# Kernel tuning notes

Measured on AMD Instinct MI355X. Metric: run time of the kernel, lower is better.

The kernel has to match this reference:

```python
import jax, jax.numpy as jnp
import numpy as np

B, S, D = 2, 1024, 2048
H, HKV, HD = 16, 8, 128
F, E, R = 5632, 8, 16
EPS = 1e-5
SCALE = 2.0  # lora_alpha / r = 32 / 16


def _rope_tables():
    pos = jnp.arange(S, dtype=jnp.float32)
    inv = 1.0 / (10000.0 ** (jnp.arange(0, HD, 2, dtype=jnp.float32) / HD))
    ang = pos[:, None] * inv[None, :]  # [S, HD/2]
    return jnp.cos(ang), jnp.sin(ang)


def setup_inputs() -> dict:
    key = jax.random.key(0)
    ks = jax.random.split(key, 18)
    p = lambda k, shp: jax.random.normal(k, shp, dtype=jnp.float32) * 0.02
    cos, sin = _rope_tables()
    return {
        'data': jax.random.normal(ks[0], (B, S, D), dtype=jnp.float32),
        'mask': jnp.zeros((1, 1, S, S), dtype=jnp.float32),
        'rope_cos': cos,
        'rope_sin': sin,
        'attn_norm_w': jnp.ones((D,), jnp.float32),
        'ffn_norm_w': jnp.ones((D,), jnp.float32),
        'wq': p(ks[1], (D, D)),
        'wk': p(ks[2], (HKV * HD, D)),
        'wv': p(ks[3], (HKV * HD, D)),
        'wo': p(ks[4], (D, D)),
        'gate_w': p(ks[5], (E, D)),
        'w1': p(ks[6], (F, D)),
        'w2': p(ks[7], (D, F)),
        'w3': p(ks[8], (F, D)),
        'w1_a': p(ks[9], (E, R, D)),
        'w1_b': p(ks[10], (E, F, R)),
        'w3_a': p(ks[11], (E, R, D)),
        'w3_b': p(ks[12], (E, F, R)),
        'w2_a': p(ks[13], (E, R, F)),
        'w2_b': p(ks[14], (E, D, R)),
    }


def _rmsnorm(x, w):
    v = jnp.mean(x.astype(jnp.float32) ** 2, axis=-1, keepdims=True)
    return (x * jax.lax.rsqrt(v + EPS)).astype(x.dtype) * w


def _rope(x, cos, sin):
    # x: [B,S,h,HD]; interleaved-pair rotation (llama apply_rotary_emb)
    x1, x2 = x[..., 0::2], x[..., 1::2]
    c, s = cos[None, :, None, :], sin[None, :, None, :]
    o1 = x1 * c - x2 * s
    o2 = x1 * s + x2 * c
    return jnp.stack([o1, o2], axis=-1).reshape(x.shape)


def reference(data, mask, rope_cos, rope_sin, attn_norm_w, ffn_norm_w,
              wq, wk, wv, wo, gate_w, w1, w2, w3,
              w1_a, w1_b, w3_a, w3_b, w2_a, w2_b):
    # ---- attention block ----
    xn = _rmsnorm(data, attn_norm_w)
    q = (xn @ wq.T).reshape(B, S, H, HD)
    k = (xn @ wk.T).reshape(B, S, HKV, HD)
    v = (xn @ wv.T).reshape(B, S, HKV, HD)
    q = _rope(q, rope_cos, rope_sin)
    k = _rope(k, rope_cos, rope_sin)
    k = jnp.repeat(k, H // HKV, axis=2)  # repeat_kv
    v = jnp.repeat(v, H // HKV, axis=2)
    scores = jnp.einsum('bqhd,bkhd->bhqk', q, k) / np.float32(np.sqrt(HD)) + mask
    probs = jax.nn.softmax(scores, axis=-1)
    attn = jnp.einsum('bhqk,bkhd->bqhd', probs, v).reshape(B, S, H * HD)
    data = data + attn @ wo.T
    # ---- MoE block ----
    sn = _rmsnorm(data, ffn_norm_w)
    logits = sn @ gate_w.T  # [B,S,E]
    # NOTE: source uses F.softmax(..., dim=1) -> softmax over SEQ axis, replicated faithfully
    rw = jax.nn.softmax(logits.astype(jnp.float32), axis=1)
    rw, sel = jax.lax.top_k(rw, 2)  # over experts (last axis)
    rw = rw / jnp.sum(rw, axis=-1, keepdims=True)
    c1 = sn @ w1.T  # [B,S,F]
    c3 = sn @ w3.T
    acc = jnp.zeros_like(data)
    for e in range(E):  # dense per-expert loop, as in source
        h1 = c1 + ((sn @ w1_a[e].T) @ w1_b[e].T) * SCALE
        h3 = c3 + ((sn @ w3_a[e].T) @ w3_b[e].T) * SCALE
        sr = jax.nn.silu(h1) * h3
        h = sr @ w2.T + ((sr @ w2_a[e].T) @ w2_b[e].T) * SCALE
        ew = jnp.sum(rw * (sel == e), axis=-1, keepdims=True).astype(h.dtype)
        acc = acc + h * ew
    return data + acc
```

## Files before the change

### kernel.cpp

```cpp
#include <hip/hip_runtime.h>
#include <hip/hip_bf16.h>
#include <stdint.h>

#define DEVI __device__ __forceinline__

typedef __attribute__((ext_vector_type(8))) short short8;
typedef __attribute__((ext_vector_type(4))) short short4b;
typedef __attribute__((ext_vector_type(4))) float f32x4;

constexpr int Bb  = 2, Ss = 1024, Dd = 2048, Hh = 16, HKVv = 8, HDd = 128;
constexpr int Ff  = 5632, Ee = 8, Rr = 16;
constexpr int Tt  = Bb * Ss;
constexpr int M2  = 2 * Tt;
constexpr int NKV = HKVv * HDd;
constexpr int NQKV = Dd + 2 * NKV;
constexpr int F2  = 2 * Ff;

DEVI unsigned short f2bf(float f) {
  union { float f; unsigned u; } x; x.f = f;
  unsigned r = (x.u + 0x7FFFu + ((x.u >> 16) & 1u)) >> 16;
  return (unsigned short)r;
}
DEVI float bf2f(unsigned short h) {
  union { unsigned u; float f; } x; x.u = ((unsigned)h) << 16; return x.f;
}
DEVI float wsum64(float v) {
  #pragma unroll
  for (int d = 1; d < 64; d <<= 1) v += __shfl_xor(v, d, 64);
  return v;
}
DEVI float wsum16(float v) {
  v += __shfl_xor(v, 1, 64); v += __shfl_xor(v, 2, 64);
  v += __shfl_xor(v, 4, 64); v += __shfl_xor(v, 8, 64);
  return v;
}
DEVI float wmax16(float v) {
  v = fmaxf(v, __shfl_xor(v, 1, 64)); v = fmaxf(v, __shfl_xor(v, 2, 64));
  v = fmaxf(v, __shfl_xor(v, 4, 64)); v = fmaxf(v, __shfl_xor(v, 8, 64));
  return v;
}
typedef __attribute__((address_space(1))) void gvoid;
typedef __attribute__((address_space(3))) void lvoid;
DEVI void gl_lds16(const void* g, void* l) {
  __builtin_amdgcn_global_load_lds((gvoid*)g, (lvoid*)l, 16, 0, 0);
}
DEVI unsigned ldsoff(const void* p) {
  return (unsigned)(uintptr_t)(lvoid*)p;
}
DEVI f32x4 mfma16x16(short8 a, short8 b, f32x4 c) {
  return __builtin_amdgcn_mfma_f32_16x16x32_bf16(a, b, c, 0, 0, 0);
}

__global__ __launch_bounds__(256) void cast_w(const float* __restrict__ in,
                                              unsigned short* __restrict__ out, int n) {
  int i = (blockIdx.x * 256 + threadIdx.x) * 8;
  if (i >= n) return;
  const float4* p = (const float4*)(in + i);
  float4 a = p[0], b = p[1];
  float v[8] = {a.x,a.y,a.z,a.w,b.x,b.y,b.z,b.w};
  short8 o;
  #pragma unroll
  for (int j = 0; j < 8; ++j) o[j] = (short)f2bf(v[j]);
  *(short8*)(out + i) = o;
}
__global__ __launch_bounds__(256) void cast_split_w(const float* __restrict__ in,
                                                    unsigned short* __restrict__ oh,
                                                    unsigned short* __restrict__ ol, int n) {
  int i = (blockIdx.x * 256 + threadIdx.x) * 8;
  if (i >= n) return;
  const float4* p = (const float4*)(in + i);
  float4 a = p[0], b = p[1];
  float v[8] = {a.x,a.y,a.z,a.w,b.x,b.y,b.z,b.w};
  short8 h, l;
  #pragma unroll
  for (int j = 0; j < 8; ++j) {
    unsigned short hb = f2bf(v[j]);
    h[j] = (short)hb;
    l[j] = (short)f2bf(v[j] - bf2f(hb));
  }
  *(short8*)(oh + i) = h;
  *(short8*)(ol + i) = l;
}
__global__ __launch_bounds__(256) void zero_f32(float* __restrict__ p, int n) {
  int i = blockIdx.x * 256 + threadIdx.x;
  if (i < n) p[i] = 0.f;
}

__global__ __launch_bounds__(256) void rmsnorm_k(const float* __restrict__ x,
                                                 const float* __restrict__ w,
                                                 unsigned short* __restrict__ out) {
  int row = blockIdx.x, tid = threadIdx.x;
  const float* xr = x + (size_t)row * Dd;
  const float4* p4 = (const float4*)(xr + tid * 8);
  float4 a = p4[0], b = p4[1];
  float v[8] = {a.x,a.y,a.z,a.w,b.x,b.y,b.z,b.w};
  float ss = 0.f;
  #pragma unroll
  for (int j = 0; j < 8; ++j) ss += v[j] * v[j];
  ss = wsum64(ss);
  __shared__ float red[4];
  int wv_ = tid >> 6, l = tid & 63;
  if (l == 0) red[wv_] = ss;
  __syncthreads();
  float tot = red[0] + red[1] + red[2] + red[3];
  float rstd = rsqrtf(tot * (1.0f / Dd) + 1e-5f);
  const float* wr = w + tid * 8;
  short8 o;
  #pragma unroll
  for (int j = 0; j < 8; ++j) o[j] = (short)f2bf(v[j] * rstd * wr[j]);
  *(short8*)(out + (size_t)row * Dd + tid * 8) = o;
}

__global__ __launch_bounds__(256) void rmsnorm_split_k(const float* __restrict__ x,
                                                       const float* __restrict__ w,
                                                       unsigned short* __restrict__ outh,
                                                       unsigned short* __restrict__ outl) {
  int row = blockIdx.x, tid = threadIdx.x;
  const float* xr = x + (size_t)row * Dd;
  const float4* p4 = (const float4*)(xr + tid * 8);
  float4 a = p4[0], b = p4[1];
  float v[8] = {a.x,a.y,a.z,a.w,b.x,b.y,b.z,b.w};
  float ss = 0.f;
  #pragma unroll
  for (int j = 0; j < 8; ++j) ss += v[j] * v[j];
  ss = wsum64(ss);
  __shared__ float red[4];
  int wv_ = tid >> 6, l = tid & 63;
  if (l == 0) red[wv_] = ss;
  __syncthreads();
  float tot = red[0] + red[1] + red[2] + red[3];
  float rstd = rsqrtf(tot * (1.0f / Dd) + 1e-5f);
  const float* wr = w + tid * 8;
  short8 oh, ol;
  #pragma unroll
  for (int j = 0; j < 8; ++j) {
    float val = v[j] * rstd * wr[j];
    unsigned short hb = f2bf(val);
    oh[j] = (short)hb;
    ol[j] = (short)f2bf(val - bf2f(hb));
  }
  *(short8*)(outh + (size_t)row * Dd + tid * 8) = oh;
  *(short8*)(outl + (size_t)row * Dd + tid * 8) = ol;
}

template <int MODE, int COLMAJ>
__global__ __launch_bounds__(512) void gemm_bt64_v3(const unsigned short* __restrict__ A,
                                                    const unsigned short* __restrict__ Bw,
                                                    void* __restrict__ C0,
                                                    void* __restrict__ C1,
                                                    int M, int N, int Kext, int ld, int gx) {
  __shared__ __align__(16) unsigned short As[128 * 64];
  __shared__ __align__(16) unsigned short Bs[128 * 64];
  int tid = threadIdx.x;
  int w = tid >> 6, l = tid & 63;
  int lr = l & 15, lg = l >> 4;
  int cpx = (int)gridDim.x >> 3;
  int bid = blockIdx.x;
  int swz = (bid & 7) * cpx + (bid >> 3);
  int mtiles = M >> 7;
  int bx, by, ks = 0;
  if (COLMAJ) { by = swz % mtiles; bx = swz / mtiles; }
  else {
    bx = swz % gx; by = swz / gx;
    if (by >= mtiles) { ks = 1; by -= mtiles; }
  }
  int m0 = by * 128, n0 = bx * 128;
  int koff = ks * Kext;
  int wr = (w >> 1) * 32, wc = (w & 1) * 64;
  f32x4 acc[2][4];
  #pragma unroll
  for (int i = 0; i < 2; ++i)
    #pragma unroll
    for (int j = 0; j < 4; ++j) acc[i][j] = (f32x4){0.f, 0.f, 0.f, 0.f};

  int srow = w * 16 + (l >> 3);
  int schunk = (l & 7) ^ (l >> 3);
  const unsigned short* ga = A  + (size_t)(m0 + srow) * ld + koff + schunk * 8;
  const unsigned short* gb = Bw + (size_t)(n0 + srow) * ld + koff + schunk * 8;
  unsigned short* lA = As + w * 1024;
  unsigned short* lB = Bs + w * 1024;

  for (int k0 = 0; k0 < Kext; k0 += 64) {
    #pragma unroll
    for (int c = 0; c < 2; ++c) {
      gl_lds16(ga + k0 + (size_t)(c * 8) * ld, lA + c * 512);
      gl_lds16(gb + k0 + (size_t)(c * 8) * ld, lB + c * 512);
    }
    __syncthreads();
    #pragma unroll
    for (int kk = 0; kk < 2; ++kk) {
      int rc = ((kk * 4 + lg) ^ (lr & 7)) * 8;
      short8 af[2], bfr[4];
      #pragma unroll
      for (int i = 0; i < 2; ++i)
        af[i]  = *(const short8*)(As + (wr + i * 16 + lr) * 64 + rc);
      #pragma unroll
      for (int j = 0; j < 4; ++j)
        bfr[j] = *(const short8*)(Bs + (wc + j * 16 + lr) * 64 + rc);
      #pragma unroll
      for (int i = 0; i < 2; ++i)
        #pragma unroll
        for (int j = 0; j < 4; ++j) acc[i][j] = mfma16x16(af[i], bfr[j], acc[i][j]);
    }
    __syncthreads();
  }
  float* Cf = (float*)(ks ? C1 : C0);
  #pragma unroll
  for (int i = 0; i < 2; ++i)
    #pragma unroll
    for (int j = 0; j < 4; ++j) {
      int m = m0 + wr + i * 16 + lg * 4;
      int n = n0 + wc + j * 16 + lr;
      #pragma unroll
      for (int r = 0; r < 4; ++r) {
        float vv = acc[i][j][r];
        size_t o = (size_t)(m + r) * N + n;
        if (MODE == 0) ((unsigned short*)C0)[o] = f2bf(vv);
        else           Cf[o] = vv;
      }
    }
}

template <int MODE, int COLMAJ>
__global__ __launch_bounds__(512) void gemm3_v3(const unsigned short* __restrict__ Ah,
                                                const unsigned short* __restrict__ Al,
                                                const unsigned short* __restrict__ Bh1,
                                                const unsigned short* __restrict__ Bl1,
                                                const unsigned short* __restrict__ Bh2,
                                                const unsigned short* __restrict__ Bl2,
                                                const unsigned short* __restrict__ Bh3,
                                                const unsigned short* __restrict__ Bl3,
                                                int nsplit1, int nsplit2,
                                                void* __restrict__ C0,
                                                const float* __restrict__ resid,
                                                int M, int N, int K, int gx) {
  __shared__ __align__(16) unsigned short Ash[128 * 32];
  __shared__ __align__(16) unsigned short Asl[128 * 32];
  __shared__ __align__(16) unsigned short Bsh[128 * 32];
  __shared__ __align__(16) unsigned short Bsl[128 * 32];
  int tid = threadIdx.x;
  int w = tid >> 6, l = tid & 63;
  int lr = l & 15, lg = l >> 4;
  int cpx = (int)gridDim.x >> 3;
  int bid = blockIdx.x;
  int swz = (bid & 7) * cpx + (bid >> 3);
  int mtiles = M >> 7;
  int bx, by;
  if (COLMAJ) { by = swz % mtiles; bx = swz / mtiles; }
  else        { bx = swz % gx;     by = swz / gx; }
  int m0 = by * 128, n0 = bx * 128;
  int wr = (w >> 1) * 32, wc = (w & 1) * 64;

  const unsigned short* Bh; const unsigned short* Bl; int nb;
  if (n0 < nsplit1)      { Bh = Bh1; Bl = Bl1; nb = n0; }
  else if (n0 < nsplit2) { Bh = Bh2; Bl = Bl2; nb = n0 - nsplit1; }
  else                   { Bh = Bh3; Bl = Bl3; nb = n0 - nsplit2; }

  f32x4 acc[2][4];
  #pragma unroll
  for (int i = 0; i < 2; ++i)
    #pragma unroll
    for (int j = 0; j < 4; ++j) acc[i][j] = (f32x4){0.f, 0.f, 0.f, 0.f};

  int srow = w * 16 + (l >> 2);
  int scol = ((l & 3) ^ ((l >> 3) & 3)) * 8;
  const unsigned short* gah = Ah + (size_t)(m0 + srow) * K + scol;
  const unsigned short* gal = Al + (size_t)(m0 + srow) * K + scol;
  const unsigned short* gbh = Bh + (size_t)(nb + srow) * K + scol;
  const unsigned short* gbl = Bl + (size_t)(nb + srow) * K + scol;
  unsigned short* lAh = Ash + w * 512;
  unsigned short* lAl = Asl + w * 512;
  unsigned short* lBh = Bsh + w * 512;
  unsigned short* lBl = Bsl + w * 512;

  for (int k0 = 0; k0 < K; k0 += 32) {
    gl_lds16(gah + k0, lAh);
    gl_lds16(gal + k0, lAl);
    gl_lds16(gbh + k0, lBh);
    gl_lds16(gbl + k0, lBl);
    __syncthreads();
    int rc = (lg ^ ((lr >> 1) & 3)) * 8;
    short8 afh[2], afl[2], bfh[4], bfl[4];
    #pragma unroll
    for (int i = 0; i < 2; ++i) {
      afh[i] = *(const short8*)(Ash + (wr + i * 16 + lr) * 32 + rc);
      afl[i] = *(const short8*)(Asl + (wr + i * 16 + lr) * 32 + rc);
    }
    #pragma unroll
    for (int j = 0; j < 4; ++j) {
      bfh[j] = *(const short8*)(Bsh + (wc + j * 16 + lr) * 32 + rc);
      bfl[j] = *(const short8*)(Bsl + (wc + j * 16 + lr) * 32 + rc);
    }
    #pragma unroll
    for (int i = 0; i < 2; ++i)
      #pragma unroll
      for (int j = 0; j < 4; ++j) {
        acc[i][j] = mfma16x16(afh[i], bfh[j], acc[i][j]);
        acc[i][j] = mfma16x16(afh[i], bfl[j], acc[i][j]);
        acc[i][j] = mfma16x16(afl[i], bfh[j], acc[i][j]);
      }
    __syncthreads();
  }
  #pragma unroll
  for (int i = 0; i < 2; ++i)
    #pragma unroll
    for (int j = 0; j < 4; ++j) {
      int m = m0 + wr + i * 16 + lg * 4;
      int n = n0 + wc + j * 16 + lr;
      #pragma unroll
      for (int r = 0; r < 4; ++r) {
        float vv = acc[i][j][r];
        size_t o = (size_t)(m + r) * N + n;
        if (MODE == 1) ((float*)C0)[o] = vv;
        else           ((float*)C0)[o] = vv + resid[o];
      }
    }
}

__global__ __launch_bounds__(128) void vsplit_k(const float* __restrict__ qkv,
                                                unsigned short* __restrict__ vh,
                                                unsigned short* __restrict__ vl) {
  int row = blockIdx.x;
  int bas = threadIdx.x * 8;
  const float4* p = (const float4*)(qkv + (size_t)row * NQKV + Dd + NKV + bas);
  float4 a = p[0], b = p[1];
  float v[8] = {a.x,a.y,a.z,a.w,b.x,b.y,b.z,b.w};
  short8 h, l;
  #pragma unroll
  for (int j = 0; j < 8; ++j) {
    unsigned short hb = f2bf(v[j]);
    h[j] = (short)hb;
    l[j] = (short)f2bf(v[j] - bf2f(hb));
  }
  size_t o = (size_t)row * NKV + bas;
  *(short8*)(vh + o) = h;
  *(short8*)(vl + o) = l;
}

__global__ void rope_split_k(const float* __restrict__ x, int xstride,
                             const float* __restrict__ cs, const float* __restrict__ sn,
                             unsigned short* __restrict__ oh, unsigned short* __restrict__ ol,
                             int nh) {
  int row = blockIdx.x;
  int s = row & (Ss - 1);
  int nelem = nh * HDd;
  int bas = threadIdx.x * 8;
  if (bas >= nelem) return;
  const float4* px = (const float4*)(x + (size_t)row * xstride + bas);
  float4 a = px[0], b = px[1];
  float vv[8] = {a.x,a.y,a.z,a.w,b.x,b.y,b.z,b.w};
  int d = bas & (HDd - 1);
  const float* cr = cs + s * 64 + (d >> 1);
  const float* sr = sn + s * 64 + (d >> 1);
  short8 hs, ls;
  #pragma unroll
  for (int p = 0; p < 4; ++p) {
    float x1 = vv[2 * p], x2 = vv[2 * p + 1];
    float c = cr[p], si = sr[p];
    float o1 = x1 * c - x2 * si;
    float o2 = x1 * si + x2 * c;
    unsigned short h1 = f2bf(o1), h2 = f2bf(o2);
    hs[2 * p] = (short)h1;      hs[2 * p + 1] = (short)h2;
    ls[2 * p] = (short)f2bf(o1 - bf2f(h1));
    ls[2 * p + 1] = (short)f2bf(o2 - bf2f(h2));
  }
  size_t o = (size_t)row * nelem + bas;
  *(short8*)(oh + o) = hs;
  *(short8*)(ol + o) = ls;
}

__global__ __launch_bounds__(256) void attn3_k(const unsigned short* __restrict__ qh,
                                               const unsigned short* __restrict__ ql,
                                               const unsigned short* __restrict__ kh,
                                               const unsigned short* __restrict__ kl,
                                               const unsigned short* __restrict__ vh,
                                               const unsigned short* __restrict__ vl,
                                               const float* __restrict__ mask,
                                               unsigned short* __restrict__ aoh,
                                               unsigned short* __restrict__ aol) {
  __shared__ __align__(16) unsigned short Ksh[32 * 128], Ksl[32 * 128];
  __shared__ __align__(16) unsigned short VTh[8 * 528], VTl[8 * 528];
  __shared__ __align__(16) unsigned short Plh[4 * 16 * 40], Pll[4 * 16 * 40];
  int tid = threadIdx.x, w = tid >> 6, l = tid & 63;
  int lr = l & 15, lg = l >> 4;
  int b = blockIdx.y >> 4, h = blockIdx.y & 15, hk = h >> 1;
  int q0 = blockIdx.x * 64 + w * 16;

  short8 qfh[4], qfl[4];
  {
    size_t qoff = ((size_t)((b * Ss + q0 + lr) * Hh + h)) * HDd;
    #pragma unroll
    for (int ds = 0; ds < 4; ++ds) {
      qfh[ds] = *(const short8*)(qh + qoff + ds * 32 + lg * 8);
      qfl[ds] = *(const short8*)(ql + qoff + ds * 32 + lg * 8);
    }
  }

  float mreg[4] = {-1e30f, -1e30f, -1e30f, -1e30f};
  float lreg[4] = {0.f, 0.f, 0.f, 0.f};
  f32x4 oacc[8];
  #pragma unroll
  for (int db = 0; db < 8; ++db) oacc[db] = (f32x4){0.f, 0.f, 0.f, 0.f};

  const float sc = 0.08838834764831845f;
  size_t kvbase = ((size_t)(b * Ss) * HKVv + hk) * HDd;
  const unsigned short* kb_h = kh + kvbase;
  const unsigned short* kb_l = kl + kvbase;
  const unsigned short* vb_h = vh + kvbase;
  const unsigned short* vb_l = vl + kvbase;

  int kc1 = (lr ^ lg) * 8;
  int kc2 = (lr ^ (lg + 4)) * 8;
  int vrow_a = w * 8 + ((l & 7) >> 1);
  int vchunk = ((l >> 3) * 2 + (l & 1)) * 8;
  unsigned short* vh1 = VTh + (2 * w) * 528;
  unsigned short* vh2 = VTh + (2 * w + 1) * 528;
  unsigned short* vl1 = VTl + (2 * w) * 528;
  unsigned short* vl2 = VTl + (2 * w + 1) * 528;
  unsigned vtbh = ldsoff(VTh) + (unsigned)lr * 8u;
  unsigned vtbl = ldsoff(VTl) + (unsigned)lr * 8u;

  for (int kv0 = 0; kv0 < Ss; kv0 += 32) {
    int r1 = kv0 + w * 8 + lg;
    gl_lds16(kb_h + (size_t)r1 * NKV + kc1,       Ksh + w * 1024);
    gl_lds16(kb_h + (size_t)(r1 + 4) * NKV + kc2, Ksh + w * 1024 + 512);
    gl_lds16(kb_l + (size_t)r1 * NKV + kc1,       Ksl + w * 1024);
    gl_lds16(kb_l + (size_t)(r1 + 4) * NKV + kc2, Ksl + w * 1024 + 512);
    int vr0 = kv0 + vrow_a;
    gl_lds16(vb_h + (size_t)vr0 * NKV + vchunk,       vh1);
    gl_lds16(vb_h + (size_t)(vr0 + 4) * NKV + vchunk, vh2);
    gl_lds16(vb_l + (size_t)vr0 * NKV + vchunk,       vl1);
    gl_lds16(vb_l + (size_t)(vr0 + 4) * NKV + vchunk, vl2);
    __syncthreads();

    f32x4 s0 = (f32x4){0.f,0.f,0.f,0.f}, s1 = (f32x4){0.f,0.f,0.f,0.f};
    #pragma unroll
    for (int ds = 0; ds < 4; ++ds) {
      int kcol = ((ds * 4 + lg) ^ (lr & 7)) * 8;
      short8 kh0 = *(const short8*)(Ksh + lr * 128 + kcol);
      short8 kh1 = *(const short8*)(Ksh + (16 + lr) * 128 + kcol);
      short8 kl0 = *(const short8*)(Ksl + lr * 128 + kcol);
      short8 kl1 = *(const short8*)(Ksl + (16 + lr) * 128 + kcol);
      s0 = mfma16x16(qfh[ds], kh0, s0);
      s0 = mfma16x16(qfh[ds], kl0, s0);
      s0 = mfma16x16(qfl[ds], kh0, s0);
      s1 = mfma16x16(qfh[ds], kh1, s1);
      s1 = mfma16x16(qfh[ds], kl1, s1);
      s1 = mfma16x16(qfl[ds], kh1, s1);
    }
    const float* mrow = mask + (size_t)(q0 + lg * 4) * Ss + kv0 + lr;
    #pragma unroll
    for (int r = 0; r < 4; ++r) {
      float a0 = s0[r] * sc + mrow[(size_t)r * Ss];
      float a1 = s1[r] * sc + mrow[(size_t)r * Ss + 16];
      float t = wmax16(fmaxf(a0, a1));
      float mn = fmaxf(mreg[r], t);
      float resc = __expf(mreg[r] - mn);
      mreg[r] = mn;
      float e0 = __expf(a0 - mn), e1 = __expf(a1 - mn);
      float ps = wsum16(e0 + e1);
      lreg[r] = lreg[r] * resc + ps;
      #pragma unroll
      for (int db = 0; db < 8; ++db) oacc[db][r] *= resc;
      unsigned short h0 = f2bf(e0), h1 = f2bf(e1);
      unsigned short* prowh = Plh + (w * 16 + lg * 4 + r) * 40;
      unsigned short* prowl = Pll + (w * 16 + lg * 4 + r) * 40;
      prowh[lr] = h0;            prowh[16 + lr] = h1;
      prowl[lr] = f2bf(e0 - bf2f(h0));
      prowl[16 + lr] = f2bf(e1 - bf2f(h1));
    }
    asm volatile("" ::: "memory");
    short8 pfh = *(const short8*)(Plh + (w * 16 + lr) * 40 + lg * 8);
    short8 pfl = *(const short8*)(Pll + (w * 16 + lr) * 40 + lg * 8);

    short4b v4[16];
    #pragma unroll
    for (int db = 0; db < 8; ++db) {
      #pragma unroll
      for (int t = 0; t < 2; ++t) {
        unsigned off = vtbh + (unsigned)((lg * 2 + t) * 1056 + db * 128);
        asm volatile("ds_read_b64_tr_b16 %0, %1" : "=v"(v4[db * 2 + t]) : "v"(off));
      }
    }
    asm volatile("s_waitcnt lgkmcnt(0)" ::: "memory");
    __builtin_amdgcn_sched_barrier(0);
    #pragma unroll
    for (int db = 0; db < 8; ++db) {
      short8 vf;
      vf[0] = v4[db*2][0]; vf[1] = v4[db*2][1]; vf[2] = v4[db*2][2]; vf[3] = v4[db*2][3];
      vf[4] = v4[db*2+1][0]; vf[5] = v4[db*2+1][1]; vf[6] = v4[db*2+1][2]; vf[7] = v4[db*2+1][3];
      oacc[db] = mfma16x16(pfh, vf, oacc[db]);
      oacc[db] = mfma16x16(pfl, vf, oacc[db]);
    }
    #pragma unroll
    for (int db = 0; db < 8; ++db) {
      #pragma unroll
      for (int t = 0; t < 2; ++t) {
        unsigned off = vtbl + (unsigned)((lg * 2 + t) * 1056 + db * 128);
        asm volatile("ds_read_b64_tr_b16 %0, %1" : "=v"(v4[db * 2 + t]) : "v"(off));
      }
    }
    asm volatile("s_waitcnt lgkmcnt(0)" ::: "memory");
    __builtin_amdgcn_sched_barrier(0);
    #pragma unroll
    for (int db = 0; db < 8; ++db) {
      short8 vf;
      vf[0] = v4[db*2][0]; vf[1] = v4[db*2][1]; vf[2] = v4[db*2][2]; vf[3] = v4[db*2][3];
      vf[4] = v4[db*2+1][0]; vf[5] = v4[db*2+1][1]; vf[6] = v4[db*2+1][2]; vf[7] = v4[db*2+1][3];
      oacc[db] = mfma16x16(pfh, vf, oacc[db]);
    }
    __syncthreads();
  }
  float inv[4];
  #pragma unroll
  for (int r = 0; r < 4; ++r) inv[r] = 1.0f / lreg[r];
  size_t obase = ((size_t)((b * Ss + q0 + lg * 4) * Hh + h)) * HDd + lr;
  #pragma unroll
  for (int db = 0; db < 8; ++db)
    #pragma unroll
    for (int r = 0; r < 4; ++r) {
      float val = oacc[db][r] * inv[r];
      unsigned short hb = f2bf(val);
      size_t o = obase + (size_t)r * Hh * HDd + db * 16;
      aoh[o] = hb;
      aol[o] = f2bf(val - bf2f(hb));
    }
}

__global__ __launch_bounds__(256) void router_logits(const float* __restrict__ x2,
                                                     const float* __restrict__ fnw,
                                                     const float* __restrict__ gw,
                                                     float* __restrict__ logits) {
  int wid = (blockIdx.x * 256 + threadIdx.x) >> 6;
  int l = threadIdx.x & 63;
  if (wid >= Tt) return;
  const float* row = x2 + (size_t)wid * Dd;
  float xs[32]; float ss = 0.f;
  #pragma unroll
  for (int c = 0; c < 32; ++c) { float t = row[c * 64 + l]; xs[c] = t; ss += t * t; }
  ss = wsum64(ss);
  float rstd = rsqrtf(ss * (1.0f / Dd) + 1e-5f);
  #pragma unroll
  for (int c = 0; c < 32; ++c) xs[c] *= rstd * fnw[c * 64 + l];
  for (int e = 0; e < 8; ++e) {
    float a = 0.f;
    #pragma unroll
    for (int c = 0; c < 32; ++c) a += xs[c] * gw[(size_t)e * Dd + c * 64 + l];
    a = wsum64(a);
    if (l == 0) logits[wid * 8 + e] = a;
  }
}
__global__ __launch_bounds__(256) void router_colstats(const float* __restrict__ logits,
                                                       float* __restrict__ mz) {
  int b = blockIdx.x >> 3, e = blockIdx.x & 7;
  int tid = threadIdx.x, wv_ = tid >> 6, l = tid & 63;
  __shared__ float red[4];
  float mx = -1e30f;
  for (int s = tid; s < Ss; s += 256) mx = fmaxf(mx, logits[(size_t)(b * Ss + s) * 8 + e]);
  #pragma unroll
  for (int d = 1; d < 64; d <<= 1) mx = fmaxf(mx, __shfl_xor(mx, d, 64));
  if (l == 0) red[wv_] = mx;
  __syncthreads();
  mx = fmaxf(fmaxf(red[0], red[1]), fmaxf(red[2], red[3]));
  __syncthreads();
  float z = 0.f;
  for (int s = tid; s < Ss; s += 256) z += expf(logits[(size_t)(b * Ss + s) * 8 + e] - mx);
  z = wsum64(z);
  if (l == 0) red[wv_] = z;
  __syncthreads();
  if (tid == 0) {
    mz[(b * 8 + e) * 2] = mx;
    mz[(b * 8 + e) * 2 + 1] = red[0] + red[1] + red[2] + red[3];
  }
}
__global__ __launch_bounds__(256) void router_select(const float* __restrict__ logits,
                                                     const float* __restrict__ mz,
                                                     int* __restrict__ sel,
                                                     float* __restrict__ ewt) {
  int t = blockIdx.x * 256 + threadIdx.x;
  if (t >= Tt) return;
  int b = t >> 10;
  float rw[8];
  #pragma unroll
  for (int e = 0; e < 8; ++e)
    rw[e] = expf(logits[(size_t)t * 8 + e] - mz[(b * 8 + e) * 2]) / mz[(b * 8 + e) * 2 + 1];
  int i0 = 0; float b0 = rw[0];
  #pragma unroll
  for (int e = 1; e < 8; ++e) if (rw[e] > b0) { b0 = rw[e]; i0 = e; }
  int i1 = -1; float b1 = -1.f;
  #pragma unroll
  for (int e = 0; e < 8; ++e) if (e != i0 && rw[e] > b1) { b1 = rw[e]; i1 = e; }
  float s = b0 + b1;
  sel[2 * t] = i0; sel[2 * t + 1] = i1;
  ewt[2 * t] = b0 / s; ewt[2 * t + 1] = b1 / s;
}
__global__ void zero_cnt_k(int* cnt) { if (threadIdx.x < 8) cnt[threadIdx.x] = 0; }
__global__ void gather_k(const int* __restrict__ sel, int* cnt, int* list) {
  int i = blockIdx.x * 256 + threadIdx.x;
  if (i >= M2) return;
  int e = sel[i];
  int pos = atomicAdd(cnt + e, 1);
  list[e * Tt + pos] = i;
}

__global__ __launch_bounds__(64) void lora_up_m(const unsigned short* __restrict__ snb,
                                                const unsigned short* __restrict__ w1ab,
                                                const unsigned short* __restrict__ w3ab,
                                                const int* __restrict__ cnt,
                                                const int* __restrict__ list,
                                                float* __restrict__ t1,
                                                float* __restrict__ t3) {
  int tile = blockIdx.x, e = blockIdx.y, ks = blockIdx.z;
  int ni = cnt[e];
  if (tile * 16 >= ni) return;
  int l = threadIdx.x, lr = l & 15, lg = l >> 4;
  int slotA = tile * 16 + lr; if (slotA >= ni) slotA = ni - 1;
  int iA = list[e * Tt + slotA];
  const unsigned short* arow = snb + (size_t)(iA >> 1) * Dd + ks * 1024;
  const unsigned short* b1 = w1ab + ((size_t)e * 16 + lr) * Dd + ks * 1024;
  const unsigned short* b3 = w3ab + ((size_t)e * 16 + lr) * Dd + ks * 1024;
  f32x4 a1 = (f32x4){0.f,0.f,0.f,0.f}, a3 = (f32x4){0.f,0.f,0.f,0.f};
  #pragma unroll 4
  for (int k0 = 0; k0 < 1024; k0 += 32) {
    short8 af  = *(const short8*)(arow + k0 + lg * 8);
    short8 b1f = *(const short8*)(b1 + k0 + lg * 8);
    short8 b3f = *(const short8*)(b3 + k0 + lg * 8);
    a1 = mfma16x16(af, b1f, a1);
    a3 = mfma16x16(af, b3f, a3);
  }
  #pragma unroll
  for (int r = 0; r < 4; ++r) {
    int slot = tile * 16 + lg * 4 + r;
    if (slot < ni) {
      int i = list[e * Tt + slot];
      atomicAdd(&t1[(size_t)i * 16 + lr], a1[r]);
      atomicAdd(&t3[(size_t)i * 16 + lr], a3[r]);
    }
  }
}

__global__ __launch_bounds__(64) void lora_down_m(const unsigned short* __restrict__ sr,
                                                  const unsigned short* __restrict__ w2ab,
                                                  const int* __restrict__ cnt,
                                                  const int* __restrict__ list,
                                                  float* __restrict__ t2) {
  int tile = blockIdx.x, e = blockIdx.y, ks = blockIdx.z;
  int ni = cnt[e];
  if (tile * 16 >= ni) return;
  int l = threadIdx.x, lr = l & 15, lg = l >> 4;
  int slotA = tile * 16 + lr; if (slotA >= ni) slotA = ni - 1;
  int iA = list[e * Tt + slotA];
  const unsigned short* arow = sr + (size_t)iA * Ff + ks * 1408;
  const unsigned short* brow = w2ab + ((size_t)e * 16 + lr) * Ff + ks * 1408;
  f32x4 acc = (f32x4){0.f,0.f,0.f,0.f};
  #pragma unroll 4
  for (int k0 = 0; k0 < 1408; k0 += 32) {
    short8 af = *(const short8*)(arow + k0 + lg * 8);
    short8 bf = *(const short8*)(brow + k0 + lg * 8);
    acc = mfma16x16(af, bf, acc);
  }
  #pragma unroll
  for (int r = 0; r < 4; ++r) {
    int slot = tile * 16 + lg * 4 + r;
    if (slot < ni) {
      int i = list[e * Tt + slot];
      atomicAdd(&t2[(size_t)i * 16 + lr], acc[r]);
    }
  }
}

__global__ __launch_bounds__(256) void expert_sr_k(const unsigned short* __restrict__ c13,
                                                   const float* __restrict__ t1,
                                                   const float* __restrict__ t3,
                                                   const float* __restrict__ w1b,
                                                   const float* __restrict__ w3b,
                                                   const int* __restrict__ cnt,
                                                   const int* __restrict__ list,
                                                   unsigned short* __restrict__ sr) {
  int e = blockIdx.y;
  int f = blockIdx.x * 256 + threadIdx.x;
  __shared__ float W1[16 * 256], W3[16 * 256];
  #pragma unroll
  for (int r = 0; r < 16; ++r) {
    W1[r * 256 + threadIdx.x] = 2.0f * w1b[((size_t)e * Ff + f) * 16 + r];
    W3[r * 256 + threadIdx.x] = 2.0f * w3b[((size_t)e * Ff + f) * 16 + r];
  }
  __syncthreads();
  int n = cnt[e];
  int chunk = (n + 7) >> 3;
  int pbeg = blockIdx.z * chunk;
  int pend = min(n, pbeg + chunk);
  for (int p = pbeg; p < pend; ++p) {
    int i = list[e * Tt + p];
    int t = i >> 1;
    const float* u1 = t1 + (size_t)i * 16;
    const float* u3 = t3 + (size_t)i * 16;
    float l1 = 0.f, l3 = 0.f;
    #pragma unroll
    for (int r = 0; r < 16; ++r) {
      l1 += u1[r] * W1[r * 256 + threadIdx.x];
      l3 += u3[r] * W3[r * 256 + threadIdx.x];
    }
    float h1 = bf2f(c13[(size_t)t * F2 + f]) + l1;
    float h3 = bf2f(c13[(size_t)t * F2 + Ff + f]) + l3;
    float sv = (h1 / (1.f + __expf(-h1))) * h3;
    sr[(size_t)i * Ff + f] = f2bf(sv);
  }
}

__global__ __launch_bounds__(256) void combine_k(const float* __restrict__ hb0,
                                                 const float* __restrict__ hb1,
                                                 const float* __restrict__ t2,
                                                 const int* __restrict__ sel,
                                                 const float* __restrict__ ewt,
                                                 const float* __restrict__ w2b,
                                                 float* __restrict__ out) {
  int t = blockIdx.x;
  int d0 = threadIdx.x * 8;
  int e0 = sel[2 * t], e1 = sel[2 * t + 1];
  float a0 = ewt[2 * t], a1 = ewt[2 * t + 1];
  float uu0[16], uu1[16];
  const float* u0 = t2 + (size_t)(2 * t) * 16;
  const float* u1 = t2 + (size_t)(2 * t + 1) * 16;
  #pragma unroll
  for (int r = 0; r < 16; ++r) { uu0[r] = u0[r]; uu1[r] = u1[r]; }
  const float* wb0 = w2b + (size_t)e0 * Dd * 16;
  const float* wb1 = w2b + (size_t)e1 * Dd * 16;
  size_t r0 = (size_t)(2 * t) * Dd, r1 = (size_t)(2 * t + 1) * Dd;
  float* orow = out + (size_t)t * Dd;
  #pragma unroll
  for (int dd = 0; dd < 8; ++dd) {
    int d = d0 + dd;
    float l0 = 0.f, l1v = 0.f;
    #pragma unroll
    for (int r = 0; r < 16; ++r) {
      l0  += uu0[r] * wb0[(size_t)d * 16 + r];
      l1v += uu1[r] * wb1[(size_t)d * 16 + r];
    }
    float h0 = hb0[r0 + d] + hb1[r0 + d];
    float h1 = hb0[r1 + d] + hb1[r1 + d];
    orow[d] += a0 * (h0 + 2.f * l0) + a1 * (h1 + 2.f * l1v);
  }
}

extern "C" void kernel_launch(void* const* d_in, const int* in_sizes, int n_in,
                              void* d_out, int out_size, void* d_ws, size_t ws_size,
                              hipStream_t stream) {
  const float* data  = (const float*)d_in[0];
  const float* mask  = (const float*)d_in[1];
  const float* ropec = (const float*)d_in[2];
  const float* ropes = (const float*)d_in[3];
  const float* anw   = (const float*)d_in[4];
  const float* fnw   = (const float*)d_in[5];
  const float* wq_f  = (const float*)d_in[6];
  const float* wk_f  = (const float*)d_in[7];
  const float* wv_f  = (const float*)d_in[8];
  const float* wo_f  = (const float*)d_in[9];
  const float* gate  = (const float*)d_in[10];
  const float* w1_f  = (const float*)d_in[11];
  const float* w2_f  = (const float*)d_in[12];
  const float* w3_f  = (const float*)d_in[13];
  const float* w1a   = (const float*)d_in[14];
  const float* w1bl  = (const float*)d_in[15];
  const float* w3a   = (const float*)d_in[16];
  const float* w3bl  = (const float*)d_in[17];
  const float* w2a   = (const float*)d_in[18];
  const float* w2bl  = (const float*)d_in[19];
  float* out = (float*)d_out;

  char* base = (char*)d_ws;
  size_t off = 0;
  auto take = [&](size_t bytes) -> char* {
    char* r = base + off;
    off += (bytes + 255) & ~(size_t)255;
    return r;
  };
  unsigned short* wqh = (unsigned short*)take((size_t)Dd * Dd * 2);
  unsigned short* wql = (unsigned short*)take((size_t)Dd * Dd * 2);
  unsigned short* wkh = (unsigned short*)take((size_t)NKV * Dd * 2);
  unsigned short* wkl = (unsigned short*)take((size_t)NKV * Dd * 2);
  unsigned short* wvh = (unsigned short*)take((size_t)NKV * Dd * 2);
  unsigned short* wvl = (unsigned short*)take((size_t)NKV * Dd * 2);
  unsigned short* woh = (unsigned short*)take((size_t)Dd * Dd * 2);
  unsigned short* wol = (unsigned short*)take((size_t)Dd * Dd * 2);
  unsigned short* w13bf = (unsigned short*)take((size_t)F2 * Dd * 2);
  unsigned short* w2bf  = (unsigned short*)take((size_t)Dd * Ff * 2);
  unsigned short* xh = (unsigned short*)take((size_t)Tt * Dd * 2);
  unsigned short* xl = (unsigned short*)take((size_t)Tt * Dd * 2);
  unsigned short* qhB = (unsigned short*)take((size_t)Tt * Dd * 2);
  unsigned short* qlB = (unsigned short*)take((size_t)Tt * Dd * 2);
  unsigned short* khB = (unsigned short*)take((size_t)Tt * NKV * 2);
  unsigned short* klB = (unsigned short*)take((size_t)Tt * NKV * 2);
  unsigned short* vhB = (unsigned short*)take((size_t)Tt * NKV * 2);
  unsigned short* vlB = (unsigned short*)take((size_t)Tt * NKV * 2);
  unsigned short* srb = (unsigned short*)take((size_t)M2 * Ff * 2);
  float* hb = (float*)take((size_t)M2 * Dd * 4);
  float* t1b = (float*)take((size_t)M2 * 16 * 4);
  float* t3b = (float*)take((size_t)M2 * 16 * 4);
  float* t2b = (float*)take((size_t)M2 * 16 * 4);
  int*   selb = (int*)take((size_t)M2 * 4);
  float* ewtb = (float*)take((size_t)M2 * 4);
  float* logitsb = (float*)take((size_t)Tt * 8 * 4);
  float* mzb = (float*)take((size_t)16 * 2 * 4);
  int*   cntb = (int*)take(8 * 4);
  int*   listb = (int*)take((size_t)8 * Tt * 4);
  unsigned short* w1ab = (unsigned short*)take((size_t)Ee * Rr * Dd * 2);
  unsigned short* w3ab = (unsigned short*)take((size_t)Ee * Rr * Dd * 2);
  unsigned short* w2ab = (unsigned short*)take((size_t)Ee * Rr * Ff * 2);
  if (off > ws_size) return;

  float* qkv = (float*)hb;
  unsigned short* aoh = xh;
  unsigned short* aol = xl;
  unsigned short* snb = qhB;
  unsigned short* c13b = wqh;
  float* hb1 = (float*)xh;

  cast_split_w<<<2048, 256, 0, stream>>>(wq_f, wqh, wql, Dd * Dd);
  cast_split_w<<<1024, 256, 0, stream>>>(wk_f, wkh, wkl, NKV * Dd);
  cast_split_w<<<1024, 256, 0, stream>>>(wv_f, wvh, wvl, NKV * Dd);
  cast_split_w<<<2048, 256, 0, stream>>>(wo_f, woh, wol, Dd * Dd);
  cast_w<<<5632, 256, 0, stream>>>(w1_f, w13bf, Ff * Dd);
  cast_w<<<5632, 256, 0, stream>>>(w3_f, w13bf + (size_t)Ff * Dd, Ff * Dd);
  cast_w<<<5632, 256, 0, stream>>>(w2_f, w2bf, Dd * Ff);
  cast_w<<<128, 256, 0, stream>>>(w1a, w1ab, Ee * Rr * Dd);
  cast_w<<<128, 256, 0, stream>>>(w3a, w3ab, Ee * Rr * Dd);
  cast_w<<<352, 256, 0, stream>>>(w2a, w2ab, Ee * Rr * Ff);
  zero_f32<<<768, 256, 0, stream>>>(t1b, 3 * M2 * 16);

  rmsnorm_split_k<<<Tt, 256, 0, stream>>>(data, anw, xh, xl);
  gemm3_v3<1, 1><<<512, 512, 0, stream>>>(xh, xl, wqh, wql, wkh, wkl, wvh, wvl,
                                          Dd, Dd + NKV, qkv, nullptr, Tt, NQKV, Dd, 32);
  vsplit_k<<<Tt, 128, 0, stream>>>(qkv, vhB, vlB);
  rope_split_k<<<Tt, 256, 0, stream>>>(qkv, NQKV, ropec, ropes, qhB, qlB, Hh);
  rope_split_k<<<Tt, 128, 0, stream>>>(qkv + Dd, NQKV, ropec, ropes, khB, klB, HKVv);
  attn3_k<<<dim3(16, 32), 256, 0, stream>>>(qhB, qlB, khB, klB, vhB, vlB, mask, aoh, aol);
  gemm3_v3<2, 1><<<256, 512, 0, stream>>>(aoh, aol, woh, wol, woh, wol, woh, wol,
                                          Dd, Dd, d_out, data, Tt, Dd, Dd, 16);

  rmsnorm_k<<<Tt, 256, 0, stream>>>(out, fnw, snb);
  router_logits<<<512, 256, 0, stream>>>(out, fnw, gate, logitsb);
  router_colstats<<<16, 256, 0, stream>>>(logitsb, mzb);
  router_select<<<8, 256, 0, stream>>>(logitsb, mzb, selb, ewtb);
  zero_cnt_k<<<1, 64, 0, stream>>>(cntb);
  gather_k<<<16, 256, 0, stream>>>(selb, cntb, listb);
  gemm_bt64_v3<0, 1><<<1408, 512, 0, stream>>>(snb, w13bf, c13b, nullptr, Tt, F2, Dd, Dd, 88);
  lora_up_m<<<dim3(128, 8, 2), 64, 0, stream>>>(snb, w1ab, w3ab, cntb, listb, t1b, t3b);
  expert_sr_k<<<dim3(22, 8, 8), 256, 0, stream>>>(c13b, t1b, t3b, w1bl, w3bl, cntb, listb, srb);
  lora_down_m<<<dim3(128, 8, 4), 64, 0, stream>>>(srb, w2ab, cntb, listb, t2b);
  gemm_bt64_v3<1, 0><<<1024, 512, 0, stream>>>(srb, w2bf, hb, hb1, M2, Dd, Ff / 2, Ff, 16);
  combine_k<<<Tt, 256, 0, stream>>>(hb, hb1, t2b, selb, ewtb, w2bl, out);
}
```

Baseline: 895.9 us.

## Double-buffer GEMM LDS tiles and fuse cast/rope/vsplit kernel launches

Both GEMM kernels now use two LDS buffers so the global-to-LDS load of the next K tile is issued before computing the current one, with one barrier per iteration instead of two. The ten weight-cast launches are merged into two multi-segment kernels, and the V split plus the Q and K RoPE kernels are merged into one 512-thread kernel; the attention indexing is changed to the new token-major Q/K/V layout. This doubles LDS use per block, which may lower occupancy, in exchange for overlapping loads with MFMA work and cutting launch overhead.

```diff
diff --git a/kernel.cpp b/kernel.cpp
--- a/kernel.cpp
+++ b/kernel.cpp
@@ -50,25 +50,17 @@
 DEVI f32x4 mfma16x16(short8 a, short8 b, f32x4 c) {
   return __builtin_amdgcn_mfma_f32_16x16x32_bf16(a, b, c, 0, 0, 0);
 }
-
-__global__ __launch_bounds__(256) void cast_w(const float* __restrict__ in,
-                                              unsigned short* __restrict__ out, int n) {
-  int i = (blockIdx.x * 256 + threadIdx.x) * 8;
-  if (i >= n) return;
-  const float4* p = (const float4*)(in + i);
+DEVI void cast8(const float* src, unsigned short* dst, size_t i) {
+  const float4* p = (const float4*)(src + i);
   float4 a = p[0], b = p[1];
   float v[8] = {a.x,a.y,a.z,a.w,b.x,b.y,b.z,b.w};
   short8 o;
   #pragma unroll
   for (int j = 0; j < 8; ++j) o[j] = (short)f2bf(v[j]);
-  *(short8*)(out + i) = o;
-}
-__global__ __launch_bounds__(256) void cast_split_w(const float* __restrict__ in,
-                                                    unsigned short* __restrict__ oh,
-                                                    unsigned short* __restrict__ ol, int n) {
-  int i = (blockIdx.x * 256 + threadIdx.x) * 8;
-  if (i >= n) return;
-  const float4* p = (const float4*)(in + i);
+  *(short8*)(dst + i) = o;
+}
+DEVI void csplit8(const float* src, unsigned short* dh, unsigned short* dl, size_t i) {
+  const float4* p = (const float4*)(src + i);
   float4 a = p[0], b = p[1];
   float v[8] = {a.x,a.y,a.z,a.w,b.x,b.y,b.z,b.w};
   short8 h, l;
@@ -78,9 +70,73 @@
     h[j] = (short)hb;
     l[j] = (short)f2bf(v[j] - bf2f(hb));
   }
-  *(short8*)(oh + i) = h;
-  *(short8*)(ol + i) = l;
-}
+  *(short8*)(dh + i) = h;
+  *(short8*)(dl + i) = l;
+}
+DEVI void rope8(const float* src, const float* cr, const float* sr,
+                unsigned short* oh, unsigned short* ol) {
+  const float4* px = (const float4*)src;
+  float4 a = px[0], b = px[1];
+  float vv[8] = {a.x,a.y,a.z,a.w,b.x,b.y,b.z,b.w};
+  short8 hs, ls;
+  #pragma unroll
+  for (int p = 0; p < 4; ++p) {
+    float x1 = vv[2 * p], x2 = vv[2 * p + 1];
+    float c = cr[p], si = sr[p];
+    float o1 = x1 * c - x2 * si;
+    float o2 = x1 * si + x2 * c;
+    unsigned short h1 = f2bf(o1), h2 = f2bf(o2);
+    hs[2 * p] = (short)h1;      hs[2 * p + 1] = (short)h2;
+    ls[2 * p] = (short)f2bf(o1 - bf2f(h1));
+    ls[2 * p + 1] = (short)f2bf(o2 - bf2f(h2));
+  }
+  *(short8*)oh = hs;
+  *(short8*)ol = ls;
+}
+
+__global__ __launch_bounds__(256) void cast_all6(const float* __restrict__ w1f,
+                                                 const float* __restrict__ w3f,
+                                                 const float* __restrict__ w2f,
+                                                 const float* __restrict__ w1a,
+                                                 const float* __restrict__ w3a,
+                                                 const float* __restrict__ w2a,
+                                                 unsigned short* __restrict__ w13,
+                                                 unsigned short* __restrict__ w2b,
+                                                 unsigned short* __restrict__ w1ab,
+                                                 unsigned short* __restrict__ w3ab,
+                                                 unsigned short* __restrict__ w2ab) {
+  int b = blockIdx.x;
+  const float* src; unsigned short* dst;
+  if (b < 5632)       { src = w1f; dst = w13; }
+  else if (b < 11264) { src = w3f; dst = w13 + (size_t)Ff * Dd; b -= 5632; }
+  else if (b < 16896) { src = w2f; dst = w2b;  b -= 11264; }
+  else if (b < 17024) { src = w1a; dst = w1ab; b -= 16896; }
+  else if (b < 17152) { src = w3a; dst = w3ab; b -= 17024; }
+  else                { src = w2a; dst = w2ab; b -= 17152; }
+  cast8(src, dst, ((size_t)b * 256 + threadIdx.x) * 8);
+}
+
+__global__ __launch_bounds__(256) void cast_split4(const float* __restrict__ wq,
+                                                   const float* __restrict__ wk,
+                                                   const float* __restrict__ wv,
+                                                   const float* __restrict__ wo,
+                                                   unsigned short* __restrict__ qh_,
+                                                   unsigned short* __restrict__ ql_,
+                                                   unsigned short* __restrict__ kh_,
+                                                   unsigned short* __restrict__ kl_,
+                                                   unsigned short* __restrict__ vh_,
+                                                   unsigned short* __restrict__ vl_,
+                                                   unsigned short* __restrict__ oh_,
+                                                   unsigned short* __restrict__ ol_) {
+  int b = blockIdx.x;
+  const float* src; unsigned short* dh; unsigned short* dl;
+  if (b < 2048)      { src = wq; dh = qh_; dl = ql_; }
+  else if (b < 3072) { src = wk; dh = kh_; dl = kl_; b -= 2048; }
+  else if (b < 4096) { src = wv; dh = vh_; dl = vl_; b -= 3072; }
+  else               { src = wo; dh = oh_; dl = ol_; b -= 4096; }
+  csplit8(src, dh, dl, ((size_t)b * 256 + threadIdx.x) * 8);
+}
+
 __global__ __launch_bounds__(256) void zero_f32(float* __restrict__ p, int n) {
   int i = blockIdx.x * 256 + threadIdx.x;
   if (i < n) p[i] = 0.f;
@@ -144,13 +200,13 @@
 }
 
 template <int MODE, int COLMAJ>
-__global__ __launch_bounds__(512) void gemm_bt64_v3(const unsigned short* __restrict__ A,
+__global__ __launch_bounds__(512) void gemm_bt64_v4(const unsigned short* __restrict__ A,
                                                     const unsigned short* __restrict__ Bw,
                                                     void* __restrict__ C0,
                                                     void* __restrict__ C1,
                                                     int M, int N, int Kext, int ld, int gx) {
-  __shared__ __align__(16) unsigned short As[128 * 64];
-  __shared__ __align__(16) unsigned short Bs[128 * 64];
+  __shared__ __align__(16) unsigned short As[2][128 * 64];
+  __shared__ __align__(16) unsigned short Bs[2][128 * 64];
   int tid = threadIdx.x;
   int w = tid >> 6, l = tid & 63;
   int lr = l & 15, lg = l >> 4;
@@ -177,33 +233,44 @@
   int schunk = (l & 7) ^ (l >> 3);
   const unsigned short* ga = A  + (size_t)(m0 + srow) * ld + koff + schunk * 8;
   const unsigned short* gb = Bw + (size_t)(n0 + srow) * ld + koff + schunk * 8;
-  unsigned short* lA = As + w * 1024;
-  unsigned short* lB = Bs + w * 1024;
-
-  for (int k0 = 0; k0 < Kext; k0 += 64) {
+
+  auto STAGE = [&](int b, int k0) {
     #pragma unroll
     for (int c = 0; c < 2; ++c) {
-      gl_lds16(ga + k0 + (size_t)(c * 8) * ld, lA + c * 512);
-      gl_lds16(gb + k0 + (size_t)(c * 8) * ld, lB + c * 512);
-    }
-    __syncthreads();
+      gl_lds16(ga + k0 + (size_t)(c * 8) * ld, As[b] + w * 1024 + c * 512);
+      gl_lds16(gb + k0 + (size_t)(c * 8) * ld, Bs[b] + w * 1024 + c * 512);
+    }
+  };
+  auto COMP = [&](int b) {
     #pragma unroll
     for (int kk = 0; kk < 2; ++kk) {
       int rc = ((kk * 4 + lg) ^ (lr & 7)) * 8;
       short8 af[2], bfr[4];
       #pragma unroll
       for (int i = 0; i < 2; ++i)
-        af[i]  = *(const short8*)(As + (wr + i * 16 + lr) * 64 + rc);
+        af[i]  = *(const short8*)(As[b] + (wr + i * 16 + lr) * 64 + rc);
       #pragma unroll
       for (int j = 0; j < 4; ++j)
-        bfr[j] = *(const short8*)(Bs + (wc + j * 16 + lr) * 64 + rc);
+        bfr[j] = *(const short8*)(Bs[b] + (wc + j * 16 + lr) * 64 + rc);
       #pragma unroll
       for (int i = 0; i < 2; ++i)
         #pragma unroll
         for (int j = 0; j < 4; ++j) acc[i][j] = mfma16x16(af[i], bfr[j], acc[i][j]);
     }
+  };
+
+  int nk = Kext >> 6;
+  STAGE(0, 0);
+  __syncthreads();
+  int cur = 0;
+  for (int kt = 0; kt < nk - 1; ++kt) {
+    STAGE(cur ^ 1, (kt + 1) << 6);
+    COMP(cur);
     __syncthreads();
-  }
+    cur ^= 1;
+  }
+  COMP(cur);
+
   float* Cf = (float*)(ks ? C1 : C0);
   #pragma unroll
   for (int i = 0; i < 2; ++i)
@@ -222,7 +289,7 @@
 }
 
 template <int MODE, int COLMAJ>
-__global__ __launch_bounds__(512) void gemm3_v3(const unsigned short* __restrict__ Ah,
+__global__ __launch_bounds__(512) void gemm3_v4(const unsigned short* __restrict__ Ah,
                                                 const unsigned short* __restrict__ Al,
                                                 const unsigned short* __restrict__ Bh1,
                                                 const unsigned short* __restrict__ Bl1,
@@ -234,10 +301,10 @@
                                                 void* __restrict__ C0,
                                                 const float* __restrict__ resid,
                                                 int M, int N, int K, int gx) {
-  __shared__ __align__(16) unsigned short Ash[128 * 32];
-  __shared__ __align__(16) unsigned short Asl[128 * 32];
-  __shared__ __align__(16) unsigned short Bsh[128 * 32];
-  __shared__ __align__(16) unsigned short Bsl[128 * 32];
+  __shared__ __align__(16) unsigned short Ash[2][128 * 32];
+  __shared__ __align__(16) unsigned short Asl[2][128 * 32];
+  __shared__ __align__(16) unsigned short Bsh[2][128 * 32];
+  __shared__ __align__(16) unsigned short Bsl[2][128 * 32];
   int tid = threadIdx.x;
   int w = tid >> 6, l = tid & 63;
   int lr = l & 15, lg = l >> 4;
@@ -268,28 +335,25 @@
   const unsigned short* gal = Al + (size_t)(m0 + srow) * K + scol;
   const unsigned short* gbh = Bh + (size_t)(nb + srow) * K + scol;
   const unsigned short* gbl = Bl + (size_t)(nb + srow) * K + scol;
-  unsigned short* lAh = Ash + w * 512;
-  unsigned short* lAl = Asl + w * 512;
-  unsigned short* lBh = Bsh + w * 512;
-  unsigned short* lBl = Bsl + w * 512;
-
-  for (int k0 = 0; k0 < K; k0 += 32) {
-    gl_lds16(gah + k0, lAh);
-    gl_lds16(gal + k0, lAl);
-    gl_lds16(gbh + k0, lBh);
-    gl_lds16(gbl + k0, lBl);
-    __syncthreads();
+
+  auto STAGE = [&](int b, int k0) {
+    gl_lds16(gah + k0, Ash[b] + w * 512);
+    gl_lds16(gal + k0, Asl[b] + w * 512);
+    gl_lds16(gbh + k0, Bsh[b] + w * 512);
+    gl_lds16(gbl + k0, Bsl[b] + w * 512);
+  };
+  auto COMP = [&](int b) {
     int rc = (lg ^ ((lr >> 1) & 3)) * 8;
     short8 afh[2], afl[2], bfh[4], bfl[4];
     #pragma unroll
     for (int i = 0; i < 2; ++i) {
-      afh[i] = *(const short8*)(Ash + (wr + i * 16 + lr) * 32 + rc);
-      afl[i] = *(const short8*)(Asl + (wr + i * 16 + lr) * 32 + rc);
+      afh[i] = *(const short8*)(Ash[b] + (wr + i * 16 + lr) * 32 + rc);
+      afl[i] = *(const short8*)(Asl[b] + (wr + i * 16 + lr) * 32 + rc);
     }
     #pragma unroll
     for (int j = 0; j < 4; ++j) {
-      bfh[j] = *(const short8*)(Bsh + (wc + j * 16 + lr) * 32 + rc);
-      bfl[j] = *(const short8*)(Bsl + (wc + j * 16 + lr) * 32 + rc);
+      bfh[j] = *(const short8*)(Bsh[b] + (wc + j * 16 + lr) * 32 + rc);
+      bfl[j] = *(const short8*)(Bsl[b] + (wc + j * 16 + lr) * 32 + rc);
     }
     #pragma unroll
     for (int i = 0; i < 2; ++i)
@@ -299,8 +363,20 @@
         acc[i][j] = mfma16x16(afh[i], bfl[j], acc[i][j]);
         acc[i][j] = mfma16x16(afl[i], bfh[j], acc[i][j]);
       }
+  };
+
+  int nk = K >> 5;
+  STAGE(0, 0);
+  __syncthreads();
+  int cur = 0;
+  for (int kt = 0; kt < nk - 1; ++kt) {
+    STAGE(cur ^ 1, (kt + 1) << 5);
+    COMP(cur);
     __syncthreads();
-  }
+    cur ^= 1;
+  }
+  COMP(cur);
+
   #pragma unroll
   for (int i = 0; i < 2; ++i)
     #pragma unroll
@@ -317,56 +393,45 @@
     }
 }
 
-__global__ __launch_bounds__(128) void vsplit_k(const float* __restrict__ qkv,
-                                                unsigned short* __restrict__ vh,
-                                                unsigned short* __restrict__ vl) {
-  int row = blockIdx.x;
-  int bas = threadIdx.x * 8;
-  const float4* p = (const float4*)(qkv + (size_t)row * NQKV + Dd + NKV + bas);
-  float4 a = p[0], b = p[1];
-  float v[8] = {a.x,a.y,a.z,a.w,b.x,b.y,b.z,b.w};
-  short8 h, l;
-  #pragma unroll
-  for (int j = 0; j < 8; ++j) {
-    unsigned short hb = f2bf(v[j]);
-    h[j] = (short)hb;
-    l[j] = (short)f2bf(v[j] - bf2f(hb));
-  }
-  size_t o = (size_t)row * NKV + bas;
-  *(short8*)(vh + o) = h;
-  *(short8*)(vl + o) = l;
-}
-
-__global__ void rope_split_k(const float* __restrict__ x, int xstride,
-                             const float* __restrict__ cs, const float* __restrict__ sn,
-                             unsigned short* __restrict__ oh, unsigned short* __restrict__ ol,
-                             int nh) {
+__global__ __launch_bounds__(512) void rope_vsplit_k(const float* __restrict__ qkv,
+                                                     const float* __restrict__ cs,
+                                                     const float* __restrict__ sn,
+                                                     unsigned short* __restrict__ qh_,
+                                                     unsigned short* __restrict__ ql_,
+                                                     unsigned short* __restrict__ kh_,
+                                                     unsigned short* __restrict__ kl_,
+                                                     unsigned short* __restrict__ vh_,
+                                                     unsigned short* __restrict__ vl_) {
   int row = blockIdx.x;
   int s = row & (Ss - 1);
-  int nelem = nh * HDd;
-  int bas = threadIdx.x * 8;
-  if (bas >= nelem) return;
-  const float4* px = (const float4*)(x + (size_t)row * xstride + bas);
-  float4 a = px[0], b = px[1];
-  float vv[8] = {a.x,a.y,a.z,a.w,b.x,b.y,b.z,b.w};
-  int d = bas & (HDd - 1);
-  const float* cr = cs + s * 64 + (d >> 1);
-  const float* sr = sn + s * 64 + (d >> 1);
-  short8 hs, ls;
-  #pragma unroll
-  for (int p = 0; p < 4; ++p) {
-    float x1 = vv[2 * p], x2 = vv[2 * p + 1];
-    float c = cr[p], si = sr[p];
-    float o1 = x1 * c - x2 * si;
-    float o2 = x1 * si + x2 * c;
-    unsigned short h1 = f2bf(o1), h2 = f2bf(o2);
-    hs[2 * p] = (short)h1;      hs[2 * p + 1] = (short)h2;
-    ls[2 * p] = (short)f2bf(o1 - bf2f(h1));
-    ls[2 * p + 1] = (short)f2bf(o2 - bf2f(h2));
-  }
-  size_t o = (size_t)row * nelem + bas;
-  *(short8*)(oh + o) = hs;
-  *(short8*)(ol + o) = ls;
+  int tid = threadIdx.x;
+  const float* base = qkv + (size_t)row * NQKV;
+  if (tid < 256) {
+    int bas = tid * 8;
+    int d = bas & (HDd - 1);
+    rope8(base + bas, cs + s * 64 + (d >> 1), sn + s * 64 + (d >> 1),
+          qh_ + (size_t)row * Dd + bas, ql_ + (size_t)row * Dd + bas);
+  } else if (tid < 384) {
+    int bas = (tid - 256) * 8;
+    int d = bas & (HDd - 1);
+    rope8(base + Dd + bas, cs + s * 64 + (d >> 1), sn + s * 64 + (d >> 1),
+          kh_ + (size_t)row * NKV + bas, kl_ + (size_t)row * NKV + bas);
+  } else {
+    int bas = (tid - 384) * 8;
+    const float4* p = (const float4*)(base + Dd + NKV + bas);
+    float4 a = p[0], b = p[1];
+    float v[8] = {a.x,a.y,a.z,a.w,b.x,b.y,b.z,b.w};
+    short8 h, l;
+    #pragma unroll
+    for (int j = 0; j < 8; ++j) {
+      unsigned short hb = f2bf(v[j]);
+      h[j] = (short)hb;
+      l[j] = (short)f2bf(v[j] - bf2f(hb));
+    }
+    size_t o = (size_t)row * NKV + bas;
+    *(short8*)(vh_ + o) = h;
+    *(short8*)(vl_ + o) = l;
+  }
 }
 
 __global__ __launch_bounds__(256) void attn3_k(const unsigned short* __restrict__ qh,
@@ -388,11 +453,11 @@
 
   short8 qfh[4], qfl[4];
   {
-    size_t qoff = ((size_t)((b * Ss + q0 + lr) * Hh + h)) * HDd;
+    size_t qoff = ((size_t)(b * Ss + q0 + lr)) * Dd;
     #pragma unroll
     for (int ds = 0; ds < 4; ++ds) {
-      qfh[ds] = *(const short8*)(qh + qoff + ds * 32 + lg * 8);
-      qfl[ds] = *(const short8*)(ql + qoff + ds * 32 + lg * 8);
+      qfh[ds] = *(const short8*)(qh + qoff + h * HDd + ds * 32 + lg * 8);
+      qfl[ds] = *(const short8*)(ql + qoff + h * HDd + ds * 32 + lg * 8);
     }
   }
 
@@ -403,7 +468,7 @@
   for (int db = 0; db < 8; ++db) oacc[db] = (f32x4){0.f, 0.f, 0.f, 0.f};
 
   const float sc = 0.08838834764831845f;
-  size_t kvbase = ((size_t)(b * Ss) * HKVv + hk) * HDd;
+  size_t kvbase = ((size_t)(b * Ss)) * NKV + hk * HDd;
   const unsigned short* kb_h = kh + kvbase;
   const unsigned short* kb_l = kl + kvbase;
   const unsigned short* vb_h = vh + kvbase;
@@ -816,26 +881,18 @@
   unsigned short* c13b = wqh;
   float* hb1 = (float*)xh;
 
-  cast_split_w<<<2048, 256, 0, stream>>>(wq_f, wqh, wql, Dd * Dd);
-  cast_split_w<<<1024, 256, 0, stream>>>(wk_f, wkh, wkl, NKV * Dd);
-  cast_split_w<<<1024, 256, 0, stream>>>(wv_f, wvh, wvl, NKV * Dd);
-  cast_split_w<<<2048, 256, 0, stream>>>(wo_f, woh, wol, Dd * Dd);
-  cast_w<<<5632, 256, 0, stream>>>(w1_f, w13bf, Ff * Dd);
-  cast_w<<<5632, 256, 0, stream>>>(w3_f, w13bf + (size_t)Ff * Dd, Ff * Dd);
-  cast_w<<<5632, 256, 0, stream>>>(w2_f, w2bf, Dd * Ff);
-  cast_w<<<128, 256, 0, stream>>>(w1a, w1ab, Ee * Rr * Dd);
-  cast_w<<<128, 256, 0, stream>>>(w3a, w3ab, Ee * Rr * Dd);
-  cast_w<<<352, 256, 0, stream>>>(w2a, w2ab, Ee * Rr * Ff);
+  cast_split4<<<6144, 256, 0, stream>>>(wq_f, wk_f, wv_f, wo_f,
+                                        wqh, wql, wkh, wkl, wvh, wvl, woh, wol);
+  cast_all6<<<17504, 256, 0, stream>>>(w1_f, w3_f, w2_f, w1a, w3a, w2a,
+                                       w13bf, w2bf, w1ab, w3ab, w2ab);
   zero_f32<<<768, 256, 0, stream>>>(t1b, 3 * M2 * 16);
 
   rmsnorm_split_k<<<Tt, 256, 0, stream>>>(data, anw, xh, xl);
-  gemm3_v3<1, 1><<<512, 512, 0, stream>>>(xh, xl, wqh, wql, wkh, wkl, wvh, wvl,
+  gemm3_v4<1, 1><<<512, 512, 0, stream>>>(xh, xl, wqh, wql, wkh, wkl, wvh, wvl,
                                           Dd, Dd + NKV, qkv, nullptr, Tt, NQKV, Dd, 32);
-  vsplit_k<<<Tt, 128, 0, stream>>>(qkv, vhB, vlB);
-  rope_split_k<<<Tt, 256, 0, stream>>>(qkv, NQKV, ropec, ropes, qhB, qlB, Hh);
-  rope_split_k<<<Tt, 128, 0, stream>>>(qkv + Dd, NQKV, ropec, ropes, khB, klB, HKVv);
+  rope_vsplit_k<<<Tt, 512, 0, stream>>>(qkv, ropec, ropes, qhB, qlB, khB, klB, vhB, vlB);
   attn3_k<<<dim3(16, 32), 256, 0, stream>>>(qhB, qlB, khB, klB, vhB, vlB, mask, aoh, aol);
-  gemm3_v3<2, 1><<<256, 512, 0, stream>>>(aoh, aol, woh, wol, woh, wol, woh, wol,
+  gemm3_v4<2, 1><<<256, 512, 0, stream>>>(aoh, aol, woh, wol, woh, wol, woh, wol,
                                           Dd, Dd, d_out, data, Tt, Dd, Dd, 16);
 
   rmsnorm_k<<<Tt, 256, 0, stream>>>(out, fnw, snb);
@@ -844,10 +901,10 @@
   router_select<<<8, 256, 0, stream>>>(logitsb, mzb, selb, ewtb);
   zero_cnt_k<<<1, 64, 0, stream>>>(cntb);
   gather_k<<<16, 256, 0, stream>>>(selb, cntb, listb);
-  gemm_bt64_v3<0, 1><<<1408, 512, 0, stream>>>(snb, w13bf, c13b, nullptr, Tt, F2, Dd, Dd, 88);
+  gemm_bt64_v4<0, 1><<<1408, 512, 0, stream>>>(snb, w13bf, c13b, nullptr, Tt, F2, Dd, Dd, 88);
   lora_up_m<<<dim3(128, 8, 2), 64, 0, stream>>>(snb, w1ab, w3ab, cntb, listb, t1b, t3b);
   expert_sr_k<<<dim3(22, 8, 8), 256, 0, stream>>>(c13b, t1b, t3b, w1bl, w3bl, cntb, listb, srb);
   lora_down_m<<<dim3(128, 8, 4), 64, 0, stream>>>(srb, w2ab, cntb, listb, t2b);
-  gemm_bt64_v3<1, 0><<<1024, 512, 0, stream>>>(srb, w2bf, hb, hb1, M2, Dd, Ff / 2, Ff, 16);
+  gemm_bt64_v4<1, 0><<<1024, 512, 0, stream>>>(srb, w2bf, hb, hb1, M2, Dd, Ff / 2, Ff, 16);
   combine_k<<<Tt, 256, 0, stream>>>(hb, hb1, t2b, selb, ewtb, w2bl, out);
 }
```

After: 878.9 us. About the same (-1.9%).
